# Kernel tuning notes

Measured on AMD Instinct MI355X. Metric: run time of the kernel, lower is better.

## Reference

```python
import jax, jax.numpy as jnp
import numpy as np
from scipy.optimize import linear_sum_assignment

B, N, K = 4, 100000, 16
EPS = 1e-6
W_CE, W_DICE = 2.0, 0.1


def setup_inputs() -> dict:
    key = jax.random.key(0)
    k1, k2, k3 = jax.random.split(key, 3)
    # predicted soft masks: probabilities over K object slots per point
    mask = jax.nn.softmax(jax.random.normal(k1, (B, N, K), dtype=jnp.float32), axis=-1)
    # ground-truth one-hot object masks
    labels = jax.random.randint(k2, (B, N), 0, K)
    gt_mask = jax.nn.one_hot(labels, K, dtype=jnp.float32)
    # per-point validity mask
    valid = (jax.random.uniform(k3, (B, N)) > 0.1).astype(jnp.float32)
    return {"mask": mask, "gt_mask": gt_mask, "valid": valid}


def _bce_terms(mask):
    m = jnp.clip(mask, EPS, 1.0 - EPS)
    return -jnp.log(m), -jnp.log1p(-m)  # cost when gt=1, cost when gt=0


def _match_cost_ce(mask, gt_mask, valid):
    # cost[b,i,j] = mean_n(valid) BCE(mask[:, :, i], gt_mask[:, :, j])
    # computed via einsum -- never materializes the (B,N,K,K) repeat of the torch code
    neg_log_m, neg_log_1m = _bce_terms(mask)
    v = valid[:, :, None]  # (B,N,1)
    pos = jnp.einsum('bni,bnj->bij', v * neg_log_m, gt_mask)
    neg = jnp.einsum('bni,bnj->bij', v * neg_log_1m, 1.0 - gt_mask)
    denom = jnp.maximum(jnp.sum(valid, axis=1), 1.0)[:, None, None]
    return (pos + neg) / denom  # (B,K,K)


def _match_cost_dice(mask, gt_mask, valid):
    v = valid[:, :, None]
    inter = jnp.einsum('bni,bnj->bij', v * mask, gt_mask)          # (B,K,K)
    sum_m = jnp.sum(v * mask, axis=1)[:, :, None]                   # (B,K,1)
    sum_g = jnp.sum(v * gt_mask, axis=1)[:, None, :]                # (B,1,K)
    return 1.0 - 2.0 * inter / (sum_m + sum_g + EPS)


def _match_mask_by_cost(cost):
    # faithful to the original: per-batch CPU Hungarian (scipy linear_sum_assignment)
    cost_np = np.asarray(jax.device_get(cost))
    n_object = cost_np.shape[-1]
    col = np.stack([linear_sum_assignment(cost_np[b], maximize=False)[1]
                    for b in range(cost_np.shape[0])], 0)
    perm = np.eye(n_object, dtype=np.float32)[col]  # (B,K,K)
    return jnp.asarray(perm)


def _ce_loss(mask, gt_mask, valid):
    neg_log_m, neg_log_1m = _bce_terms(mask)
    bce = gt_mask * neg_log_m + (1.0 - gt_mask) * neg_log_1m  # (B,N,K)
    v = valid[:, :, None]
    return jnp.sum(bce * v) / (jnp.maximum(jnp.sum(valid), 1.0) * mask.shape[-1])


def _dice_loss(mask, gt_mask, valid):
    v = valid[:, :, None]
    inter = jnp.sum(v * mask * gt_mask, axis=1)                     # (B,K)
    denom = jnp.sum(v * mask, axis=1) + jnp.sum(v * gt_mask, axis=1)
    return jnp.mean(1.0 - 2.0 * inter / (denom + EPS))


def reference(mask, gt_mask, valid):
    # 1) matching cost on detached predictions (gradients never flow through matching)
    m_det = jax.lax.stop_gradient(mask)
    cost = W_CE * _match_cost_ce(m_det, gt_mask, valid) \
         + W_DICE * _match_cost_dice(m_det, gt_mask, valid)
    # 2) Hungarian matching -> permutation (B,K,K)
    perm = _match_mask_by_cost(cost)
    # 3) permute gt slots, detach
    gt_perm = jax.lax.stop_gradient(jnp.einsum('bij,bnj->bni', perm, gt_mask))
    # 4) weighted CE + Dice loss
    l_ce = _ce_loss(mask, gt_perm, valid)
    l_dice = _dice_loss(mask, gt_perm, valid)
    loss = W_CE * l_ce + W_DICE * l_dice
    return loss
```

## Files before the change

kernel.cpp:

```cpp
#include <hip/hip_runtime.h>

#define NBATCH 4
#define NROWS  100000
#define KD     16
#define EPSF   1e-6f
#define WCE    2.0f
#define WDICE  0.1f
#define NREP   8
#define LN2F   0.6931471805599453f
#define SRS    272

typedef __attribute__((ext_vector_type(8))) short short8;
typedef __attribute__((ext_vector_type(4))) float f32x4;

__device__ __forceinline__ unsigned short bf16rne(float x) {
  unsigned u = __float_as_uint(x);
  unsigned r = u + 0x7FFFu + ((u >> 16) & 1u);
  return (unsigned short)(r >> 16);
}

__device__ __forceinline__ void async_copy16(const float* g, float* l) {
  __builtin_amdgcn_global_load_lds(
      (const __attribute__((address_space(1))) float*)g,
      (__attribute__((address_space(3))) float*)l, 16, 0, 0);
}

__global__ __launch_bounds__(256, 4) void sml_accum(
    const float* __restrict__ mask, const float* __restrict__ gt,
    const float* __restrict__ valid, float* __restrict__ ws)
{
  const int b    = blockIdx.y;
  const int tid  = (int)threadIdx.x;
  const int lane = tid & 63;
  const int wv   = tid >> 6;
  const int q    = lane >> 4;
  const int c    = lane & 15;
  const int row0 = blockIdx.x * 256;

  __shared__ float sBuf[9216];
  float* sM = sBuf;
  float* sG = sBuf + 16 * SRS;

  const float* maskb  = mask  + (size_t)b * NROWS * KD;
  const float* gtb    = gt    + (size_t)b * NROWS * KD;
  const float* validb = valid + (size_t)b * NROWS;

#pragma unroll
  for (int i = 0; i < 4; ++i) {
    const int g   = i * 256 + tid;
    const int rg  = row0 + (g >> 2);
    const int rc  = (rg < NROWS) ? rg : (NROWS - 1);
    const size_t off = (size_t)rc * KD + (size_t)(g & 3) * 4;
    const int dst = (g >> 6) * SRS + (g & 63) * 4;
    async_copy16(maskb + off, &sM[dst]);
    async_copy16(gtb   + off, &sG[dst]);
  }

  float vv[2][8];
#pragma unroll
  for (int ch = 0; ch < 2; ++ch) {
    const int grow = row0 + wv * 64 + ch * 32 + 8 * q;
    if (grow + 7 < NROWS) {
      const float4 va  = *(const float4*)(validb + grow);
      const float4 vb4 = *(const float4*)(validb + grow + 4);
      vv[ch][0] = va.x;  vv[ch][1] = va.y;  vv[ch][2] = va.z;  vv[ch][3] = va.w;
      vv[ch][4] = vb4.x; vv[ch][5] = vb4.y; vv[ch][6] = vb4.z; vv[ch][7] = vb4.w;
    } else {
#pragma unroll
      for (int t = 0; t < 8; ++t)
        vv[ch][t] = (grow + t < NROWS) ? validb[grow + t] : 0.f;
    }
  }
  __syncthreads();

  f32x4 accP = {0.f, 0.f, 0.f, 0.f};
  f32x4 accQ = {0.f, 0.f, 0.f, 0.f};
  f32x4 accI = {0.f, 0.f, 0.f, 0.f};

#pragma unroll
  for (int ch = 0; ch < 2; ++ch) {
    const int rt = wv * 64 + ch * 32 + 8 * q;
    float m[8], g[8];
#pragma unroll
    for (int t = 0; t < 8; ++t) {
      const int r = rt + t;
      const int a = (r >> 4) * SRS + (r & 15) * 16 + c;
      m[t] = sM[a];
      g[t] = sG[a];
    }

    short8 fP, fQ, fI, fB;
#pragma unroll
    for (int t = 0; t < 8; ++t) {
      const float mc = fminf(fmaxf(m[t], EPSF), 1.f - EPSF);
      const float lm = __log2f(mc);
      const float l1 = __log2f(1.f - mc);
      fP[t] = (short)bf16rne(LN2F * (l1 - lm));
      fQ[t] = (short)bf16rne(-LN2F * l1);
      fI[t] = (short)bf16rne(m[t]);
      fB[t] = (short)bf16rne(vv[ch][t] * g[t]);
    }
    accP = __builtin_amdgcn_mfma_f32_16x16x32_bf16(fP, fB, accP, 0, 0, 0);
    accQ = __builtin_amdgcn_mfma_f32_16x16x32_bf16(fQ, fB, accQ, 0, 0, 0);
    accI = __builtin_amdgcn_mfma_f32_16x16x32_bf16(fI, fB, accI, 0, 0, 0);
  }

  __syncthreads();
#pragma unroll
  for (int r = 0; r < 4; ++r) {
    const int idx = (4 * q + r) * 16 + c;
    sBuf[wv * 768 + idx]        = accP[r];
    sBuf[3072 + wv * 768 + idx] = accQ[r];
    sBuf[6144 + wv * 768 + idx] = accI[r];
  }
  __syncthreads();

  const int rep = (int)blockIdx.x & (NREP - 1);
  float* wsb = ws + ((size_t)rep * NBATCH + b) * 768;
  {
    float sP = 0.f, sQ = 0.f, sI = 0.f;
#pragma unroll
    for (int wvv = 0; wvv < 4; ++wvv) {
      sP += sBuf[wvv * 768 + tid];
      sQ += sBuf[3072 + wvv * 768 + tid];
      sI += sBuf[6144 + wvv * 768 + tid];
    }
    unsafeAtomicAdd(&wsb[tid],       sP);
    unsafeAtomicAdd(&wsb[256 + tid], sQ);
    unsafeAtomicAdd(&wsb[512 + tid], sI);
  }
}

#define DPP_U(x, C) ((unsigned)__builtin_amdgcn_update_dpp(0, (int)(x), (C), 0xF, 0xF, true))

__device__ __forceinline__ float rowsum16(float x) {
  x += __uint_as_float(DPP_U(__float_as_uint(x), 0x128));
  x += __uint_as_float(DPP_U(__float_as_uint(x), 0x124));
  x += __uint_as_float(DPP_U(__float_as_uint(x), 0x122));
  x += __uint_as_float(DPP_U(__float_as_uint(x), 0x121));
  return x;
}
__device__ __forceinline__ unsigned rowmin16(unsigned x) {
  unsigned y;
  y = DPP_U(x, 0x128); x = (y < x) ? y : x;
  y = DPP_U(x, 0x124); x = (y < x) ? y : x;
  y = DPP_U(x, 0x122); x = (y < x) ? y : x;
  y = DPP_U(x, 0x121); x = (y < x) ? y : x;
  return x;
}
__device__ __forceinline__ float readlane_f(float x, int l) {
  return __int_as_float(__builtin_amdgcn_readlane(__float_as_int(x), l));
}
__device__ __forceinline__ int rfl(int x) { return __builtin_amdgcn_readfirstlane(x); }

__device__ __forceinline__ float sel16v(int idx,
  float x0, float x1, float x2, float x3, float x4, float x5, float x6, float x7,
  float x8, float x9, float x10, float x11, float x12, float x13, float x14, float x15)
{
  const float a0 = (idx & 1) ? x1  : x0;
  const float a1 = (idx & 1) ? x3  : x2;
  const float a2 = (idx & 1) ? x5  : x4;
  const float a3 = (idx & 1) ? x7  : x6;
  const float a4 = (idx & 1) ? x9  : x8;
  const float a5 = (idx & 1) ? x11 : x10;
  const float a6 = (idx & 1) ? x13 : x12;
  const float a7 = (idx & 1) ? x15 : x14;
  const float b0 = (idx & 2) ? a1 : a0;
  const float b1 = (idx & 2) ? a3 : a2;
  const float b2 = (idx & 2) ? a5 : a4;
  const float b3 = (idx & 2) ? a7 : a6;
  const float c0 = (idx & 4) ? b1 : b0;
  const float c1 = (idx & 4) ? b3 : b2;
  return (idx & 8) ? c1 : c0;
}

#define R16(M) M(0) M(1) M(2) M(3) M(4) M(5) M(6) M(7) M(8) M(9) M(10) M(11) M(12) M(13) M(14) M(15)
#define SEL16(p, idx) sel16v(idx, p##0,p##1,p##2,p##3,p##4,p##5,p##6,p##7,p##8,p##9,p##10,p##11,p##12,p##13,p##14,p##15)

#define LD3(i)  const float pc##i = sB[i*16 + col]; \
                const float qc##i = sB[256 + i*16 + col]; \
                const float ic##i = sB[512 + i*16 + col];
#define SGQS(i) sg += ic##i; qs += qc##i;
#define MKA(i)  const float Sm##i = rowsum16(ic##i); \
  const float a##i = WCE * (pc##i + rowsum16(qc##i)) / Vb \
                   + WDICE * (1.f - 2.f * ic##i / (Sm##i + sg + EPSF));
#define PKA(i)  const unsigned t##i = (__float_as_uint(a##i + 64.f) & 0xFFFFFFF0u) | (unsigned)i;

__global__ __launch_bounds__(256, 1) void sml_solve(const float* __restrict__ ws,
                                                    float* __restrict__ out)
{
  const int tid = (int)threadIdx.x;
  const int w   = tid >> 6;
  const int l   = tid & 63;
  const int col = l & 15;
  __shared__ float sAcc[NBATCH][768];
  __shared__ float part[NBATCH][3];

  float* sB = sAcc[w];
#pragma unroll
  for (int k = 0; k < 3; ++k) {
    const int idx4 = k * 64 + l;
    float4 s = {0.f, 0.f, 0.f, 0.f};
#pragma unroll
    for (int r = 0; r < NREP; ++r) {
      const float4 t = *(const float4*)(ws + ((size_t)r * NBATCH + w) * 768 + idx4 * 4);
      s.x += t.x; s.y += t.y; s.z += t.z; s.w += t.w;
    }
    *(float4*)&sB[idx4 * 4] = s;
  }
  __syncthreads();

  R16(LD3)
  float sg = 0.f, qs = 0.f;
  R16(SGQS)
  const float V    = rowsum16(sg);
  const float Vb   = fmaxf(V, 1.f);
  const float Btot = rowsum16(qs);
  R16(MKA)

  R16(PKA)
  unsigned mA, mB2, mC2, mD2;
  {
    const unsigned s0 = t0  < t1  ? t0  : t1;
    const unsigned s1 = t2  < t3  ? t2  : t3;
    const unsigned s2 = t4  < t5  ? t4  : t5;
    const unsigned s3 = t6  < t7  ? t6  : t7;
    const unsigned s4 = t8  < t9  ? t8  : t9;
    const unsigned s5 = t10 < t11 ? t10 : t11;
    const unsigned s6 = t12 < t13 ? t12 : t13;
    const unsigned s7 = t14 < t15 ? t14 : t15;
    mA  = s0 < s1 ? s0 : s1;
    mB2 = s2 < s3 ? s2 : s3;
    mC2 = s4 < s5 ? s4 : s5;
    mD2 = s6 < s7 ? s6 : s7;
  }
  const unsigned mAB  = mA  < mB2 ? mA  : mB2;
  const unsigned mCD  = mC2 < mD2 ? mC2 : mD2;
  const unsigned mall = mAB < mCD ? mAB : mCD;
  const int r0i = (int)(mall & 15u);
  float vdual = SEL16(a, r0i);

  unsigned long long pword = 0ull;
  unsigned pmask = 0u;
  unsigned rowused = 0u;
#pragma unroll
  for (int j = 0; j < 16; ++j) {
    const int rj = __builtin_amdgcn_readlane(r0i, j);
    if (!((rowused >> rj) & 1u)) {
      rowused |= 1u << rj;
      pmask   |= 1u << j;
      pword   |= (unsigned long long)rj << (4 * j);
    }
  }

  float u_t = 0.f;

  for (int i = 0; i < 16; ++i) {
    if ((rowused >> i) & 1u) continue;
    float minv = 1e30f;
    int   way  = -1;
    bool  used = false;
    float Dent = 0.f;
    float Dcum = 0.f;
    bool  intree = (col == i);
    int   i0 = i;
    int   j0 = -1;

    for (int it = 0; it < 17; ++it) {
      const float u0  = readlane_f(u_t, i0);
      const float cur = SEL16(a, i0) - u0 - vdual;
      if (!used && cur < minv) { minv = cur; way = j0; }
      unsigned pk = (__float_as_uint((used ? 1e30f : minv) + 64.f) & 0xFFFFFFF0u)
                  | (unsigned)col;
      pk = rowmin16(pk);
      const float delta = __uint_as_float(pk & 0xFFFFFFF0u) - 64.f;
      if (used) vdual -= delta; else minv -= delta;
      Dcum += delta;
      const int j1s = rfl((int)(pk & 15u));
      const int  pj1 = rfl((int)((pword >> (4 * j1s)) & 15ull));
      const bool asg = (pmask >> j1s) & 1u;
      j0 = j1s;
      if (!asg) break;
      used   = used   || (col == j1s);
      Dent   = (col == pj1) ? Dcum : Dent;
      intree = intree || (col == pj1);
      i0 = pj1;
    }
    u_t += intree ? (Dcum - Dent) : 0.f;

    int jcur = rfl(j0);
    for (int s = 0; s < 17; ++s) {
      const int wy   = rfl(__builtin_amdgcn_readlane(way, jcur));
      const int prev = (wy >= 0) ? (int)((pword >> (4 * wy)) & 15ull) : i;
      pword = (pword & ~(15ull << (4 * jcur)))
            | ((unsigned long long)prev << (4 * jcur));
      pmask |= 1u << jcur;
      if (wy < 0) break;
      jcur = rfl(wy);
    }
  }

  const int ri  = (int)((pword >> (4 * col)) & 15ull);
  const float pcm = SEL16(pc, ri);
  const float icm = SEL16(ic, ri);
  const float smv = SEL16(Sm, ri);
  const float cce = rowsum16(pcm);
  const float dce = rowsum16(1.f - 2.f * icm / (smv + sg + EPSF));
  if (l == 0) { part[w][0] = cce + Btot; part[w][1] = dce; part[w][2] = V; }
  __syncthreads();

  if (tid == 0) {
    float C = 0.f, D = 0.f, Vt = 0.f;
#pragma unroll
    for (int bb = 0; bb < NBATCH; ++bb) {
      C += part[bb][0]; D += part[bb][1]; Vt += part[bb][2];
    }
    Vt = fmaxf(Vt, 1.f);
    out[0] = WCE * C / (Vt * (float)KD) + WDICE * D / 64.f;
  }
}

extern "C" void kernel_launch(void* const* d_in, const int* in_sizes, int n_in,
                              void* d_out, int out_size, void* d_ws, size_t ws_size,
                              hipStream_t stream)
{
  (void)in_sizes; (void)n_in; (void)out_size; (void)ws_size;
  const float* mask  = (const float*)d_in[0];
  const float* gt    = (const float*)d_in[1];
  const float* valid = (const float*)d_in[2];
  float* out = (float*)d_out;
  float* ws  = (float*)d_ws;

  hipMemsetAsync(d_ws, 0, (size_t)NREP * NBATCH * 768 * sizeof(float), stream);

  dim3 grid((NROWS + 255) / 256, NBATCH);
  sml_accum<<<grid, 256, 0, stream>>>(mask, gt, valid, ws);
  sml_solve<<<1, 256, 0, stream>>>(ws, out);
}
```

Measured before the change: 102.4 us.

## Add auction-style augmenting pre-pass before Hungarian and drop redundant barrier

Inserts a bounded row-reduction/auction pre-pass (up to 24 steps) that assigns unmatched rows by comparing the best and second-best reduced costs, adjusting column duals, and displacing previous owners. The aim is to leave fewer rows for the serial Dijkstra-style Hungarian loop, which iterates once per unmatched row. It also removes a __syncthreads after the per-wave LDS reduction, since each wave only reads its own slice. This adds extra warp-reduction work up front and depends on the dual updates staying consistent with the later phase.

```diff
diff --git a/kernel.cpp b/kernel.cpp
--- a/kernel.cpp
+++ b/kernel.cpp
@@ -208,7 +208,6 @@
     }
     *(float4*)&sB[idx4 * 4] = s;
   }
-  __syncthreads();
 
   R16(LD3)
   float sg = 0.f, qs = 0.f;
@@ -254,6 +253,43 @@
   }
 
   float u_t = 0.f;
+
+  {
+    int steps = 24;
+    for (int i = 0; i < 16 && steps > 0; ++i) {
+      if ((rowused >> i) & 1u) continue;
+      int icur = i;
+      while (steps-- > 0) {
+        const float d = SEL16(a, icur) - vdual;
+        unsigned pk1 = (__float_as_uint(d + 64.f) & 0xFFFFFFF0u) | (unsigned)col;
+        const unsigned m1 = rowmin16(pk1);
+        const int j1 = rfl((int)(m1 & 15u));
+        const unsigned pk2 = (col == j1) ? 0xFFFFFFFFu : pk1;
+        const unsigned m2 = rowmin16(pk2);
+        const int j2 = rfl((int)(m2 & 15u));
+        const float d1 = readlane_f(d, j1);
+        const float d2 = readlane_f(d, j2);
+        const bool strict = d1 < d2;
+        int jt = j1;
+        if (strict) {
+          if (col == j1) vdual -= (d2 - d1);
+        } else {
+          const bool occ1 = (pmask >> j1) & 1u;
+          const bool occ2 = (pmask >> j2) & 1u;
+          if (occ1 && !occ2) jt = j2;
+        }
+        if (col == icur) u_t = d2;
+        const bool occ = (pmask >> jt) & 1u;
+        const int owner = occ ? (int)((pword >> (4 * jt)) & 15ull) : -1;
+        pword = (pword & ~(15ull << (4 * jt)))
+              | ((unsigned long long)icur << (4 * jt));
+        pmask   |= 1u << jt;
+        rowused |= 1u << icur;
+        if (owner >= 0) { rowused &= ~(1u << owner); icur = owner; }
+        else break;
+      }
+    }
+  }
 
   for (int i = 0; i < 16; ++i) {
     if ((rowused >> i) & 1u) continue;
```

New measurement: 106.7 us. 4.2% more time.
